# Kernel tuning notes

Measured on AMD Instinct MI355X. Metric: run time of the kernel, lower is better.

Reference implementation:

```python
import jax, jax.numpy as jnp
import numpy as np

B, S, D = 4, 4096, 1024
H, DH, F = 16, 64, 64
DFF = 4096
EPS_LN = 1e-5
EPS_ATTN = 1e-6


def setup_inputs() -> dict:
    key = jax.random.key(0)
    ks = jax.random.split(key, 12)
    s = 1.0 / np.sqrt(D)
    inp = {
        'x': jax.random.normal(ks[0], (B, S, D), dtype=jnp.float32),
        'ln1_g': jnp.ones((D,), jnp.float32),
        'ln1_b': jnp.zeros((D,), jnp.float32),
        'wq': jax.random.normal(ks[1], (D, H * DH), jnp.float32) * s,
        'wk': jax.random.normal(ks[2], (D, H * DH), jnp.float32) * s,
        'wv': jax.random.normal(ks[3], (D, H * DH), jnp.float32) * s,
        'proj': jax.random.normal(ks[4], (DH, F), jnp.float32) / np.sqrt(F),
        'wo': jax.random.normal(ks[5], (H * DH, D), jnp.float32) * s,
        'bo': jnp.zeros((D,), jnp.float32),
        'ln2_g': jnp.ones((D,), jnp.float32),
        'ln2_b': jnp.zeros((D,), jnp.float32),
        'w1': jax.random.normal(ks[6], (D, DFF), jnp.float32) * s,
        'b1': jnp.zeros((DFF,), jnp.float32),
        'w2': jax.random.normal(ks[7], (DFF, D), jnp.float32) / np.sqrt(DFF),
        'b2': jnp.zeros((D,), jnp.float32),
    }
    return inp


def _layernorm(x, g, b):
    mu = jnp.mean(x, axis=-1, keepdims=True)
    var = jnp.mean(jnp.square(x - mu), axis=-1, keepdims=True)
    return (x - mu) * jax.lax.rsqrt(var + EPS_LN) * g + b


def _heads(t):  # [B,S,H*DH] -> [B,H,S,DH]
    return t.reshape(B, S, H, DH).transpose(0, 2, 1, 3)


def _feature_map(t, proj):  # [B,H,S,DH] -> [B,H,S,F]
    return jax.nn.relu(jnp.einsum('bhnd,df->bhnf', t, proj)) + EPS_ATTN


def reference(x, ln1_g, ln1_b, wq, wk, wv, proj, wo, bo, ln2_g, ln2_b, w1, b1, w2, b2):
    h = _layernorm(x, ln1_g, ln1_b)
    q = _feature_map(_heads(h @ wq), proj)
    k = _feature_map(_heads(h @ wk), proj)
    v = _heads(h @ wv)
    kv = jnp.einsum('bhnf,bhnd->bhfd', k, v)          # [B,H,F,DH]
    k_sum = k.sum(axis=-2)                            # [B,H,F]
    num = jnp.einsum('bhnf,bhfd->bhnd', q, kv)        # [B,H,S,DH]
    den = jnp.einsum('bhnf,bhf->bhn', q, k_sum) + EPS_ATTN
    attn = num / den[..., None]
    attn = attn.transpose(0, 2, 1, 3).reshape(B, S, H * DH)
    x = x + attn @ wo + bo
    h2 = _layernorm(x, ln2_g, ln2_b)
    ffn = jax.nn.gelu(h2 @ w1 + b1, approximate=False) @ w2 + b2
    return x + ffn
```

## Files before the change

### kernel.cpp

```cpp
#include <hip/hip_runtime.h>
#include <hip/hip_bf16.h>
#include <math.h>

using bf16 = __hip_bfloat16;
typedef __attribute__((ext_vector_type(8))) short short8;
typedef __attribute__((ext_vector_type(4))) float f32x4;

constexpr int Bc = 4, Sc = 4096, Dc = 1024, Hc = 16, DHc = 64, Fc = 64, DFFc = 4096;
constexpr float EPS_LN_C = 1e-5f, EPS_ATTN_C = 1e-6f;
constexpr int KVSPLIT = 16;

static __device__ __forceinline__ float b2f(bf16 v) { return __bfloat162float(v); }
static __device__ __forceinline__ bf16 f2b(float f) { return __float2bfloat16(f); }

__device__ float block_reduce_sum(float v) {
  __shared__ float red[4];
  int lane = threadIdx.x & 63, wid = threadIdx.x >> 6;
#pragma unroll
  for (int off = 32; off > 0; off >>= 1) v += __shfl_down(v, off, 64);
  __syncthreads();
  if (lane == 0) red[wid] = v;
  __syncthreads();
  return red[0] + red[1] + red[2] + red[3];
}

__global__ void ln_kernel(const float* __restrict__ x, const float* __restrict__ g,
                          const float* __restrict__ bta, bf16* __restrict__ out) {
  int row = blockIdx.x;
  const float* xr = x + (size_t)row * Dc;
  int t = threadIdx.x;
  float v[4];
#pragma unroll
  for (int i = 0; i < 4; ++i) v[i] = xr[t + 256 * i];
  float s = block_reduce_sum(v[0] + v[1] + v[2] + v[3]);
  float mu = s * (1.f / Dc);
  float vs = 0.f;
#pragma unroll
  for (int i = 0; i < 4; ++i) { float d = v[i] - mu; vs += d * d; }
  vs = block_reduce_sum(vs);
  float rstd = rsqrtf(vs * (1.f / Dc) + EPS_LN_C);
  bf16* orow = out + (size_t)row * Dc;
#pragma unroll
  for (int i = 0; i < 4; ++i) {
    int c = t + 256 * i;
    orow[c] = f2b((v[i] - mu) * rstd * g[c] + bta[c]);
  }
}

__global__ void tcvt_kernel(const float* __restrict__ in, bf16* __restrict__ out,
                            int K, int N) {
  __shared__ float t[32][33];
  int n0 = blockIdx.x * 32, k0 = blockIdx.y * 32;
  int tid = threadIdx.x;
#pragma unroll
  for (int i = 0; i < 4; ++i) {
    int idx = tid + 256 * i;
    int r = idx >> 5, c = idx & 31;
    t[r][c] = in[(size_t)(k0 + r) * N + n0 + c];
  }
  __syncthreads();
#pragma unroll
  for (int i = 0; i < 4; ++i) {
    int idx = tid + 256 * i;
    int r = idx >> 5, c = idx & 31;
    out[(size_t)(n0 + r) * K + k0 + c] = f2b(t[c][r]);
  }
}


template <int EPI>
__global__ __launch_bounds__(512, 2)
void mgemm256_kernel(const ushort* __restrict__ A, const ushort* __restrict__ Bt,
                     const float* __restrict__ bias, const float* __restrict__ res,
                     float* __restrict__ outF, bf16* __restrict__ outB,
                     int M, int N, int K, int lda, int ldbt) {
  constexpr int SLOT = 256 * 32;
  __shared__ ushort AsR[4][SLOT];
  __shared__ ushort BsR[4][SLOT];
  const int tid = threadIdx.x;
  const int wave = tid >> 6, lane = tid & 63;
  const int wr = wave >> 2, wc = wave & 3;
  const int mrow = lane & 15, quad = lane >> 4;

  int nn = gridDim.x, nm = gridDim.y;
  int bid = blockIdx.y * nn + blockIdx.x;
  int mtile, ntile;
  if ((nm & 7) == 0) {
    int xcd = bid & 7, s = bid >> 3;
    int mpx = nm >> 3;
    int mloc = s / nn;
    ntile = s - mloc * nn;
    mtile = xcd * mpx + mloc;
  } else { mtile = blockIdx.y; ntile = blockIdx.x; }
  const int row0 = mtile * 256, col0 = ntile * 256;

  const int srowL = tid >> 2;
  const int sOff = (((tid & 3) ^ ((tid >> 3) & 3)) << 3);
  const ushort* aB = A + (size_t)(row0 + srowL) * lda + sOff;
  const ushort* bB = Bt + (size_t)(col0 + srowL) * ldbt + sOff;
  const int dst = tid * 8;

  auto stage = [&](int sg, int l) {
    const int sl = sg & 3;
    __builtin_amdgcn_global_load_lds(
        (const __attribute__((address_space(1))) void*)(aB + (size_t)(l * 128) * lda + sg * 32),
        (__attribute__((address_space(3))) void*)(&AsR[sl][l * 4096 + dst]), 16, 0, 0);
    __builtin_amdgcn_global_load_lds(
        (const __attribute__((address_space(1))) void*)(bB + (size_t)(l * 128) * ldbt + sg * 32),
        (__attribute__((address_space(3))) void*)(&BsR[sl][l * 4096 + dst]), 16, 0, 0);
  };

  const int cq = (quad << 3) ^ (((mrow >> 1) & 3) << 3);

  f32x4 acc[8][4] = {};
  const int NS = K >> 5;

  stage(0, 0); stage(0, 1); stage(1, 0); stage(1, 1); stage(2, 0); stage(2, 1);
  asm volatile("s_waitcnt vmcnt(8)" ::: "memory");
  __builtin_amdgcn_s_barrier();

  for (int sg = 0; sg < NS; ++sg) {
    const ushort* As_ = &AsR[sg & 3][0];
    const ushort* Bs_ = &BsR[sg & 3][0];
    short8 afv[4], bfv[4];
#pragma unroll
    for (int i2 = 0; i2 < 4; ++i2)
      afv[i2] = *(const short8*)(As_ + (wr * 128 + i2 * 16 + mrow) * 32 + cq);
#pragma unroll
    for (int n = 0; n < 4; ++n)
      bfv[n] = *(const short8*)(Bs_ + (wc * 64 + (n >> 1) * 32 + (n & 1) * 16 + mrow) * 32 + cq);
    if (sg + 3 < NS) stage(sg + 3, 0);
    __builtin_amdgcn_sched_barrier(0);
    __builtin_amdgcn_s_barrier();
    asm volatile("s_waitcnt lgkmcnt(0)" ::: "memory");
    __builtin_amdgcn_sched_barrier(0);
    __builtin_amdgcn_s_setprio(1);
#pragma unroll
    for (int i2 = 0; i2 < 4; ++i2)
#pragma unroll
      for (int n = 0; n < 4; ++n)
        acc[i2][n] = __builtin_amdgcn_mfma_f32_16x16x32_bf16(afv[i2], bfv[n], acc[i2][n], 0, 0, 0);
    __builtin_amdgcn_s_setprio(0);
    __builtin_amdgcn_sched_barrier(0);
    __builtin_amdgcn_s_barrier();
#pragma unroll
    for (int i2 = 0; i2 < 4; ++i2)
      afv[i2] = *(const short8*)(As_ + (wr * 128 + 64 + i2 * 16 + mrow) * 32 + cq);
    if (sg + 3 < NS) stage(sg + 3, 1);
    __builtin_amdgcn_sched_barrier(0);
    __builtin_amdgcn_s_barrier();
    asm volatile("s_waitcnt lgkmcnt(0)" ::: "memory");
    __builtin_amdgcn_sched_barrier(0);
    __builtin_amdgcn_s_setprio(1);
#pragma unroll
    for (int i2 = 0; i2 < 4; ++i2)
#pragma unroll
      for (int n = 0; n < 4; ++n)
        acc[4 + i2][n] = __builtin_amdgcn_mfma_f32_16x16x32_bf16(afv[i2], bfv[n], acc[4 + i2][n], 0, 0, 0);
    __builtin_amdgcn_s_setprio(0);
    if (sg + 1 < NS) {
      if (sg + 3 < NS)      asm volatile("s_waitcnt vmcnt(8)" ::: "memory");
      else if (sg + 2 < NS) asm volatile("s_waitcnt vmcnt(4)" ::: "memory");
      else                  asm volatile("s_waitcnt vmcnt(0)" ::: "memory");
    }
    __builtin_amdgcn_sched_barrier(0);
    __builtin_amdgcn_s_barrier();
  }

#pragma unroll
  for (int i = 0; i < 8; ++i) {
#pragma unroll
    for (int j = 0; j < 4; ++j) {
      int rb = row0 + wr * 128 + i * 16 + quad * 4;
      int c = col0 + wc * 64 + j * 16 + mrow;
#pragma unroll
      for (int r = 0; r < 4; ++r) {
        int rr = rb + r;
        float v = acc[i][j][r];
        if (EPI == 1 || EPI == 2) v += bias[c];
        if (EPI == 3) { if (bias) v += bias[c]; }
        if (EPI == 2) v = 0.5f * v * (1.f + erff(v * 0.70710678118654752f));
        if (EPI == 1 || EPI == 3) v += res[(size_t)rr * N + c];
        if (EPI == 4) {
          outB[((size_t)(c >> 10) * (size_t)(Bc * Sc) + rr) * 1024 + (c & 1023)] = f2b(v);
        } else if (EPI == 0 || EPI == 2) {
          outB[(size_t)rr * N + c] = f2b(v);
        } else {
          outF[(size_t)rr * N + c] = v;
        }
      }
    }
  }
}

__global__ __launch_bounds__(256, 2)
void fm_mfma(const ushort* __restrict__ qin, const ushort* __restrict__ pjt,
             bf16* __restrict__ qf) {
  __shared__ ushort As[256 * 64];
  __shared__ ushort Bs[64 * 64];
  int t = threadIdx.x;
  int wave = t >> 6, lane = t & 63;
  int mrow = lane & 15, quad = lane >> 4;
  int b = blockIdx.z, h = blockIdx.y, s0 = blockIdx.x * 256;
  const ushort* abase = qin + ((size_t)b * Sc + s0) * (Hc * DHc) + h * DHc;

#pragma unroll
  for (int i = 0; i < 8; ++i) {
    int c = t + 256 * i;
    int row = c >> 3, col = (c & 7) * 8;
    __builtin_amdgcn_global_load_lds(
        (const __attribute__((address_space(1))) void*)(abase + (size_t)row * (Hc * DHc) + col),
        (__attribute__((address_space(3))) void*)(As + c * 8), 16, 0, 0);
  }
#pragma unroll
  for (int i = 0; i < 2; ++i) {
    int c = t + 256 * i;
    __builtin_amdgcn_global_load_lds(
        (const __attribute__((address_space(1))) void*)(pjt + c * 8),
        (__attribute__((address_space(3))) void*)(Bs + c * 8), 16, 0, 0);
  }
  __syncthreads();

  f32x4 acc[4][4] = {};
#pragma unroll
  for (int step = 0; step < 2; ++step) {
    short8 af[4], bfv[4];
#pragma unroll
    for (int i = 0; i < 4; ++i)
      af[i] = *(const short8*)(As + (wave * 64 + i * 16 + mrow) * 64 + quad * 8 + step * 32);
#pragma unroll
    for (int j = 0; j < 4; ++j)
      bfv[j] = *(const short8*)(Bs + (j * 16 + mrow) * 64 + quad * 8 + step * 32);
#pragma unroll
    for (int i = 0; i < 4; ++i)
#pragma unroll
      for (int j = 0; j < 4; ++j)
        acc[i][j] = __builtin_amdgcn_mfma_f32_16x16x32_bf16(af[i], bfv[j], acc[i][j], 0, 0, 0);
  }

  size_t obase = ((size_t)(b * Hc + h)) * Sc + s0;
#pragma unroll
  for (int i = 0; i < 4; ++i) {
#pragma unroll
    for (int j = 0; j < 4; ++j) {
      int f = j * 16 + mrow;
#pragma unroll
      for (int r = 0; r < 4; ++r) {
        int s = wave * 64 + i * 16 + quad * 4 + r;
        float v = fmaxf(acc[i][j][r], 0.f) + EPS_ATTN_C;
        qf[(obase + s) * Fc + f] = f2b(v);
      }
    }
  }
}

__global__ __launch_bounds__(256, 2)
void kvp_mfma(const ushort* __restrict__ kf, const ushort* __restrict__ v,
              float* __restrict__ kvp, float* __restrict__ ksump) {
  constexpr int LT = 72;
  __shared__ ushort kfT[64 * LT];
  __shared__ ushort vT[64 * LT];
  int t = threadIdx.x;
  int wave = t >> 6, lane = t & 63;
  int mrow = lane & 15, quad = lane >> 4;
  int split = blockIdx.x, bh = blockIdx.y;
  int b = bh >> 4, h = bh & 15;
  int sbase = split * (Sc / KVSPLIT);

  short8 ones, zero;
#pragma unroll
  for (int i = 0; i < 8; ++i) { ones[i] = (short)0x3F80; zero[i] = 0; }
  short8 bks = (mrow == 0) ? ones : zero;

  f32x4 acc[4] = {};
  f32x4 accks = {};

  for (int sc = 0; sc < Sc / KVSPLIT; sc += 64) {
    __syncthreads();
    int sl = t >> 2, c8 = (t & 3) * 8;
    const ushort* kp = kf + (((size_t)bh * Sc) + sbase + sc + sl) * Fc + c8;
    const ushort* vp = v + (((size_t)b * Sc) + sbase + sc + sl) * (Hc * DHc) + h * DHc + c8;
#pragma unroll
    for (int half = 0; half < 2; ++half) {
      short8 kv8 = *(const short8*)(kp + half * 32);
      short8 vv8 = *(const short8*)(vp + half * 32);
#pragma unroll
      for (int jj = 0; jj < 8; ++jj) {
        kfT[(c8 + half * 32 + jj) * LT + sl] = (ushort)kv8[jj];
        vT[(c8 + half * 32 + jj) * LT + sl] = (ushort)vv8[jj];
      }
    }
    __syncthreads();
#pragma unroll
    for (int step = 0; step < 2; ++step) {
      short8 af = *(const short8*)(kfT + (wave * 16 + mrow) * LT + quad * 8 + step * 32);
      short8 bfv[4];
#pragma unroll
      for (int j = 0; j < 4; ++j)
        bfv[j] = *(const short8*)(vT + (j * 16 + mrow) * LT + quad * 8 + step * 32);
#pragma unroll
      for (int j = 0; j < 4; ++j)
        acc[j] = __builtin_amdgcn_mfma_f32_16x16x32_bf16(af, bfv[j], acc[j], 0, 0, 0);
      accks = __builtin_amdgcn_mfma_f32_16x16x32_bf16(af, bks, accks, 0, 0, 0);
    }
  }

  size_t pbase = (size_t)bh * KVSPLIT + split;
#pragma unroll
  for (int j = 0; j < 4; ++j) {
    int d = j * 16 + mrow;
#pragma unroll
    for (int r = 0; r < 4; ++r) {
      int f = wave * 16 + quad * 4 + r;
      kvp[(pbase * 64 + f) * 64 + d] = acc[j][r];
    }
  }
  if (mrow == 0) {
#pragma unroll
    for (int r = 0; r < 4; ++r) {
      int f = wave * 16 + quad * 4 + r;
      ksump[pbase * 64 + f] = accks[r];
    }
  }
}

__global__ void kvr_kernel(const float* __restrict__ kvp, const float* __restrict__ ksump,
                           bf16* __restrict__ kvt, bf16* __restrict__ ksum16) {
  int bh = blockIdx.x;
  int t = threadIdx.x;
#pragma unroll
  for (int i = 0; i < 16; ++i) {
    int idx = t + 256 * i;
    int f = idx >> 6, d = idx & 63;
    float s = 0.f;
#pragma unroll
    for (int j = 0; j < KVSPLIT; ++j)
      s += kvp[((size_t)bh * KVSPLIT + j) * 4096 + idx];
    kvt[((size_t)bh * 64 + d) * 64 + f] = f2b(s);
  }
  if (t < 64) {
    float s = 0.f;
#pragma unroll
    for (int j = 0; j < KVSPLIT; ++j)
      s += ksump[((size_t)bh * KVSPLIT + j) * 64 + t];
    ksum16[bh * 64 + t] = f2b(s);
  }
}

__global__ __launch_bounds__(256, 2)
void attn_mfma(const ushort* __restrict__ qf, const ushort* __restrict__ kvt,
               const ushort* __restrict__ ksum16, bf16* __restrict__ attn) {
  __shared__ ushort As[256 * 64];
  __shared__ ushort Bs[64 * 64];
  int t = threadIdx.x;
  int wave = t >> 6, lane = t & 63;
  int mrow = lane & 15, quad = lane >> 4;
  int b = blockIdx.z, h = blockIdx.y, s0 = blockIdx.x * 256;
  int bh = b * Hc + h;
  const ushort* abase = qf + (((size_t)bh * Sc) + s0) * Fc;
  const ushort* bbase = kvt + (size_t)bh * 4096;

#pragma unroll
  for (int i = 0; i < 8; ++i) {
    int c = t + 256 * i;
    __builtin_amdgcn_global_load_lds(
        (const __attribute__((address_space(1))) void*)(abase + c * 8),
        (__attribute__((address_space(3))) void*)(As + c * 8), 16, 0, 0);
  }
#pragma unroll
  for (int i = 0; i < 2; ++i) {
    int c = t + 256 * i;
    __builtin_amdgcn_global_load_lds(
        (const __attribute__((address_space(1))) void*)(bbase + c * 8),
        (__attribute__((address_space(3))) void*)(Bs + c * 8), 16, 0, 0);
  }
  short8 zero;
#pragma unroll
  for (int i = 0; i < 8; ++i) zero[i] = 0;
  short8 ksf[2];
#pragma unroll
  for (int step = 0; step < 2; ++step) {
    short8 kv8 = *(const short8*)(ksum16 + bh * 64 + quad * 8 + step * 32);
    ksf[step] = (mrow == 0) ? kv8 : zero;
  }
  __syncthreads();

  f32x4 acc[4][4] = {};
  f32x4 accd[4] = {};
#pragma unroll
  for (int step = 0; step < 2; ++step) {
    short8 af[4], bfv[4];
#pragma unroll
    for (int i = 0; i < 4; ++i)
      af[i] = *(const short8*)(As + (wave * 64 + i * 16 + mrow) * 64 + quad * 8 + step * 32);
#pragma unroll
    for (int j = 0; j < 4; ++j)
      bfv[j] = *(const short8*)(Bs + (j * 16 + mrow) * 64 + quad * 8 + step * 32);
#pragma unroll
    for (int i = 0; i < 4; ++i) {
#pragma unroll
      for (int j = 0; j < 4; ++j)
        acc[i][j] = __builtin_amdgcn_mfma_f32_16x16x32_bf16(af[i], bfv[j], acc[i][j], 0, 0, 0);
      accd[i] = __builtin_amdgcn_mfma_f32_16x16x32_bf16(af[i], ksf[step], accd[i], 0, 0, 0);
    }
  }

#pragma unroll
  for (int i = 0; i < 4; ++i) {
    float inv[4];
#pragma unroll
    for (int r = 0; r < 4; ++r) {
      float den = __shfl(accd[i][r], lane & 48);
      inv[r] = 1.0f / (den + EPS_ATTN_C);
    }
#pragma unroll
    for (int j = 0; j < 4; ++j) {
      int d = j * 16 + mrow;
#pragma unroll
      for (int r = 0; r < 4; ++r) {
        int s = s0 + wave * 64 + i * 16 + quad * 4 + r;
        attn[((size_t)(b * Sc + s)) * (Hc * DHc) + h * DHc + d] = f2b(acc[i][j][r] * inv[r]);
      }
    }
  }
}

extern "C" void kernel_launch(void* const* d_in, const int* in_sizes, int n_in,
                              void* d_out, int out_size, void* d_ws, size_t ws_size,
                              hipStream_t stream) {
  const float* x     = (const float*)d_in[0];
  const float* ln1_g = (const float*)d_in[1];
  const float* ln1_b = (const float*)d_in[2];
  const float* wq    = (const float*)d_in[3];
  const float* wk    = (const float*)d_in[4];
  const float* wv    = (const float*)d_in[5];
  const float* proj  = (const float*)d_in[6];
  const float* wo    = (const float*)d_in[7];
  const float* bo    = (const float*)d_in[8];
  const float* ln2_g = (const float*)d_in[9];
  const float* ln2_b = (const float*)d_in[10];
  const float* w1    = (const float*)d_in[11];
  const float* b1    = (const float*)d_in[12];
  const float* w2    = (const float*)d_in[13];
  const float* b2    = (const float*)d_in[14];
  float* out = (float*)d_out;
  (void)ws_size; (void)in_sizes; (void)n_in; (void)out_size;

  const size_t TOK = (size_t)Bc * Sc;
  const size_t REG = TOK * Dc * sizeof(bf16);
  char* ws = (char*)d_ws;
  bf16* R0 = (bf16*)(ws + 0 * REG);
  bf16* R1 = (bf16*)(ws + 1 * REG);
  bf16* R2 = (bf16*)(ws + 2 * REG);
  bf16* R3 = (bf16*)(ws + 3 * REG);
  bf16* mid = R1;
  float* kvpart = (float*)R2;
  float* kspart = (float*)((char*)R2 + (size_t)64 * KVSPLIT * 4096 * 4);
  char* p = ws + 4 * REG;
  bf16* kvt   = (bf16*)p;                 p += (size_t)64 * 64 * 64 * 2;
  bf16* ksb16 = (bf16*)p;                 p += (size_t)64 * 64 * 2;
  bf16* pjt   = (bf16*)p;                 p += (size_t)64 * 64 * 2;
  bf16* wqt = (bf16*)p;                   p += (size_t)Dc * Dc * 2;
  bf16* wkt = (bf16*)p;                   p += (size_t)Dc * Dc * 2;
  bf16* wvt = (bf16*)p;                   p += (size_t)Dc * Dc * 2;
  bf16* wot = (bf16*)p;                   p += (size_t)Dc * Dc * 2;
  bf16* w1t = (bf16*)p;                   p += (size_t)Dc * DFFc * 2;
  bf16* w2t = (bf16*)p;                   p += (size_t)Dc * DFFc * 2;

  dim3 blk(256);
  dim3 blk512(512);
  tcvt_kernel<<<dim3(Dc / 32, Dc / 32), blk, 0, stream>>>(wq, wqt, Dc, Dc);
  tcvt_kernel<<<dim3(Dc / 32, Dc / 32), blk, 0, stream>>>(wk, wkt, Dc, Dc);
  tcvt_kernel<<<dim3(Dc / 32, Dc / 32), blk, 0, stream>>>(wv, wvt, Dc, Dc);
  tcvt_kernel<<<dim3(Dc / 32, Dc / 32), blk, 0, stream>>>(wo, wot, Dc, Dc);
  tcvt_kernel<<<dim3(DFFc / 32, Dc / 32), blk, 0, stream>>>(w1, w1t, Dc, DFFc);
  tcvt_kernel<<<dim3(Dc / 32, DFFc / 32), blk, 0, stream>>>(w2, w2t, DFFc, Dc);
  tcvt_kernel<<<dim3(2, 2), blk, 0, stream>>>(proj, pjt, 64, 64);

  ln_kernel<<<dim3(TOK), blk, 0, stream>>>(x, ln1_g, ln1_b, R0);

  dim3 gQKV(3072 / 256, TOK / 256);
  mgemm256_kernel<4><<<gQKV, blk512, 0, stream>>>((const ushort*)R0, (const ushort*)wqt,
                                                  nullptr, nullptr, nullptr, R1,
                                                  TOK, 3072, Dc, Dc, Dc);

  dim3 gF(Sc / 256, Hc, Bc);
  fm_mfma<<<gF, blk, 0, stream>>>((const ushort*)R1, (const ushort*)pjt, R0);
  fm_mfma<<<gF, blk, 0, stream>>>((const ushort*)R2, (const ushort*)pjt, R1);

  kvp_mfma<<<dim3(KVSPLIT, Bc * Hc), blk, 0, stream>>>((const ushort*)R1, (const ushort*)R3,
                                                       kvpart, kspart);
  kvr_kernel<<<dim3(Bc * Hc), blk, 0, stream>>>(kvpart, kspart, kvt, ksb16);

  attn_mfma<<<gF, blk, 0, stream>>>((const ushort*)R0, (const ushort*)kvt,
                                    (const ushort*)ksb16, R2);

  dim3 gD(Dc / 256, TOK / 256);
  mgemm256_kernel<1><<<gD, blk512, 0, stream>>>((const ushort*)R2, (const ushort*)wot, bo, x,
                                                out, nullptr, TOK, Dc, Dc, Dc, Dc);

  ln_kernel<<<dim3(TOK), blk, 0, stream>>>(out, ln2_g, ln2_b, R0);

  dim3 gW1(2048 / 256, TOK / 256);
  mgemm256_kernel<2><<<gW1, blk512, 0, stream>>>((const ushort*)R0, (const ushort*)w1t, b1, nullptr,
                                                 nullptr, mid, TOK, 2048, Dc, Dc, Dc);
  mgemm256_kernel<3><<<gD, blk512, 0, stream>>>((const ushort*)mid, (const ushort*)w2t, b2, out,
                                                out, nullptr, TOK, Dc, 2048, 2048, DFFc);
  mgemm256_kernel<2><<<gW1, blk512, 0, stream>>>((const ushort*)R0, (const ushort*)(w1t + (size_t)2048 * Dc), b1 + 2048,
                                                 nullptr, nullptr, mid, TOK, 2048, Dc, Dc, Dc);
  mgemm256_kernel<3><<<gD, blk512, 0, stream>>>((const ushort*)mid, (const ushort*)(w2t + 2048), nullptr, out,
                                                out, nullptr, TOK, Dc, 2048, 2048, DFFc);
}
```

Baseline: 885.5 us.

## Double-buffer LDS fragments in registers and use one barrier per k-step

Restructures the bf16 GEMM main loop. Each k-step now reads all A and B fragments for the next stage into a second register buffer while the MFMAs for the current stage run. This replaces the earlier split half-tile scheme, which had four barriers and explicit lgkmcnt waits per iteration. The aim is to hide LDS read latency and cut synchronisation, at the cost of roughly 96 extra VGPRs for the fragment buffers, and it assumes an even number of k-steps.

```diff
diff --git a/kernel.cpp b/kernel.cpp
--- a/kernel.cpp
+++ b/kernel.cpp
@@ -100,71 +100,64 @@
   const ushort* bB = Bt + (size_t)(col0 + srowL) * ldbt + sOff;
   const int dst = tid * 8;
 
-  auto stage = [&](int sg, int l) {
+  auto stage = [&](int sg) {
     const int sl = sg & 3;
-    __builtin_amdgcn_global_load_lds(
-        (const __attribute__((address_space(1))) void*)(aB + (size_t)(l * 128) * lda + sg * 32),
-        (__attribute__((address_space(3))) void*)(&AsR[sl][l * 4096 + dst]), 16, 0, 0);
-    __builtin_amdgcn_global_load_lds(
-        (const __attribute__((address_space(1))) void*)(bB + (size_t)(l * 128) * ldbt + sg * 32),
-        (__attribute__((address_space(3))) void*)(&BsR[sl][l * 4096 + dst]), 16, 0, 0);
+#pragma unroll
+    for (int l = 0; l < 2; ++l) {
+      __builtin_amdgcn_global_load_lds(
+          (const __attribute__((address_space(1))) void*)(aB + (size_t)(l * 128) * lda + sg * 32),
+          (__attribute__((address_space(3))) void*)(&AsR[sl][l * 4096 + dst]), 16, 0, 0);
+      __builtin_amdgcn_global_load_lds(
+          (const __attribute__((address_space(1))) void*)(bB + (size_t)(l * 128) * ldbt + sg * 32),
+          (__attribute__((address_space(3))) void*)(&BsR[sl][l * 4096 + dst]), 16, 0, 0);
+    }
   };
 
   const int cq = (quad << 3) ^ (((mrow >> 1) & 3) << 3);
+  const int arow = wr * 128 + mrow;
+  const int brow = wc * 64 + mrow;
 
   f32x4 acc[8][4] = {};
   const int NS = K >> 5;
 
-  stage(0, 0); stage(0, 1); stage(1, 0); stage(1, 1); stage(2, 0); stage(2, 1);
+  short8 fx[12], fy[12];
+
+  auto dsread = [&](int sl, short8 (&f)[12]) {
+    const ushort* As_ = &AsR[sl][0];
+    const ushort* Bs_ = &BsR[sl][0];
+#pragma unroll
+    for (int i = 0; i < 8; ++i)
+      f[i] = *(const short8*)(As_ + (arow + i * 16) * 32 + cq);
+#pragma unroll
+    for (int j = 0; j < 4; ++j)
+      f[8 + j] = *(const short8*)(Bs_ + (brow + j * 16) * 32 + cq);
+  };
+
+  auto iter = [&](int s, short8 (&cur)[12], short8 (&nxt)[12]) {
+    if (s + 2 < NS) asm volatile("s_waitcnt vmcnt(4)" ::: "memory");
+    else            asm volatile("s_waitcnt vmcnt(0)" ::: "memory");
+    __builtin_amdgcn_s_barrier();
+    asm volatile("" ::: "memory");
+    if (s + 3 < NS) stage(s + 3);
+    if (s + 1 < NS) dsread((s + 1) & 3, nxt);
+    __builtin_amdgcn_s_setprio(1);
+#pragma unroll
+    for (int i = 0; i < 8; ++i)
+#pragma unroll
+      for (int j = 0; j < 4; ++j)
+        acc[i][j] = __builtin_amdgcn_mfma_f32_16x16x32_bf16(cur[i], cur[8 + j], acc[i][j], 0, 0, 0);
+    __builtin_amdgcn_s_setprio(0);
+  };
+
+  stage(0); stage(1); stage(2);
   asm volatile("s_waitcnt vmcnt(8)" ::: "memory");
   __builtin_amdgcn_s_barrier();
-
-  for (int sg = 0; sg < NS; ++sg) {
-    const ushort* As_ = &AsR[sg & 3][0];
-    const ushort* Bs_ = &BsR[sg & 3][0];
-    short8 afv[4], bfv[4];
-#pragma unroll
-    for (int i2 = 0; i2 < 4; ++i2)
-      afv[i2] = *(const short8*)(As_ + (wr * 128 + i2 * 16 + mrow) * 32 + cq);
-#pragma unroll
-    for (int n = 0; n < 4; ++n)
-      bfv[n] = *(const short8*)(Bs_ + (wc * 64 + (n >> 1) * 32 + (n & 1) * 16 + mrow) * 32 + cq);
-    if (sg + 3 < NS) stage(sg + 3, 0);
-    __builtin_amdgcn_sched_barrier(0);
-    __builtin_amdgcn_s_barrier();
-    asm volatile("s_waitcnt lgkmcnt(0)" ::: "memory");
-    __builtin_amdgcn_sched_barrier(0);
-    __builtin_amdgcn_s_setprio(1);
-#pragma unroll
-    for (int i2 = 0; i2 < 4; ++i2)
-#pragma unroll
-      for (int n = 0; n < 4; ++n)
-        acc[i2][n] = __builtin_amdgcn_mfma_f32_16x16x32_bf16(afv[i2], bfv[n], acc[i2][n], 0, 0, 0);
-    __builtin_amdgcn_s_setprio(0);
-    __builtin_amdgcn_sched_barrier(0);
-    __builtin_amdgcn_s_barrier();
-#pragma unroll
-    for (int i2 = 0; i2 < 4; ++i2)
-      afv[i2] = *(const short8*)(As_ + (wr * 128 + 64 + i2 * 16 + mrow) * 32 + cq);
-    if (sg + 3 < NS) stage(sg + 3, 1);
-    __builtin_amdgcn_sched_barrier(0);
-    __builtin_amdgcn_s_barrier();
-    asm volatile("s_waitcnt lgkmcnt(0)" ::: "memory");
-    __builtin_amdgcn_sched_barrier(0);
-    __builtin_amdgcn_s_setprio(1);
-#pragma unroll
-    for (int i2 = 0; i2 < 4; ++i2)
-#pragma unroll
-      for (int n = 0; n < 4; ++n)
-        acc[4 + i2][n] = __builtin_amdgcn_mfma_f32_16x16x32_bf16(afv[i2], bfv[n], acc[4 + i2][n], 0, 0, 0);
-    __builtin_amdgcn_s_setprio(0);
-    if (sg + 1 < NS) {
-      if (sg + 3 < NS)      asm volatile("s_waitcnt vmcnt(8)" ::: "memory");
-      else if (sg + 2 < NS) asm volatile("s_waitcnt vmcnt(4)" ::: "memory");
-      else                  asm volatile("s_waitcnt vmcnt(0)" ::: "memory");
-    }
-    __builtin_amdgcn_sched_barrier(0);
-    __builtin_amdgcn_s_barrier();
+  asm volatile("" ::: "memory");
+  dsread(0, fx);
+
+  for (int s = 0; s < NS; s += 2) {
+    iter(s, fx, fy);
+    iter(s + 1, fy, fx);
   }
 
 #pragma unroll
```

New measurement: 942.4 us. 1.06x slower.
